# Kernel optimization log

Hardware: AMD Instinct MI355X
Metric: run time of the kernel (lower is better)

Reference implementation:

```python
import jax, jax.numpy as jnp
import numpy as np

DIM_MODEL = 1024
NUM_HEADS = 16
HEAD_DIM = DIM_MODEL // NUM_HEADS
NEG = -1000000000.0


def setup_inputs() -> dict:
    key = jax.random.key(0)
    ks = jax.random.split(key, 11)
    B, S, D = 2, 2048, DIM_MODEL
    s = 1.0 / np.sqrt(D)
    return {
        "q": jax.random.normal(ks[0], (B, S, D), jnp.float32),
        "k": jax.random.normal(ks[1], (B, S, D), jnp.float32),
        "v": jax.random.normal(ks[2], (B, S, D), jnp.float32),
        "Wq": jax.random.normal(ks[3], (D, D), jnp.float32) * s,
        "bq": jnp.zeros((D,), jnp.float32),
        "Wk": jax.random.normal(ks[4], (D, D), jnp.float32) * s,
        "bk": jnp.zeros((D,), jnp.float32),
        "Wv": jax.random.normal(ks[5], (D, D), jnp.float32) * s,
        "bv": jnp.zeros((D,), jnp.float32),
        "Wo": jax.random.normal(ks[6], (D, D), jnp.float32) * s,
        "bo": jnp.zeros((D,), jnp.float32),
    }


def reference(q, k, v, Wq, bq, Wk, bk, Wv, bv, Wo, bo):
    B, S, D = q.shape
    H, hd = NUM_HEADS, HEAD_DIM

    def proj(x, W, b):
        # torch Linear: x @ W.T + b, then split heads -> [B, H, S, hd]
        y = jnp.einsum("bsd,ed->bse", x, W) + b
        return y.reshape(B, S, H, hd).transpose(0, 2, 1, 3)

    qh = proj(q, Wq, bq)
    kh = proj(k, Wk, bk)
    vh = proj(v, Wv, bv)

    scores = jnp.einsum("bhqd,bhkd->bhqk", qh, kh) / np.sqrt(hd)
    # torch.triu(ones(S,S), diagonal=0): upper triangle INCLUDING diagonal is masked
    mask = jnp.triu(jnp.ones((S, S), bool))
    scores = jnp.where(mask, NEG, scores)
    # softmax over dim=-2 (query axis), as in the original module
    attn = jax.nn.softmax(scores, axis=-2)
    ctx = jnp.einsum("bhqk,bhkd->bhqd", attn, vh)  # [B,H,S,hd]
    ctx = ctx.transpose(0, 2, 1, 3).reshape(B, S, D)
    return jnp.einsum("bsd,ed->bse", ctx, Wo) + bo
```

## Files before the change

kernel.cpp:

```cpp
#include <hip/hip_runtime.h>

typedef __bf16 bf16;
typedef __attribute__((ext_vector_type(8))) __bf16 bf16x8;
typedef __attribute__((ext_vector_type(2))) __bf16 bf16x2;
typedef __attribute__((ext_vector_type(4))) float f32x4;

#define AS1 __attribute__((address_space(1)))
#define AS3 __attribute__((address_space(3)))

#define BB 2
#define SS 2048
#define DD 1024
#define HH 16
#define HD 64
#define BH (BB*HH)

#define QSCALE 0.1803368801111244f

static __device__ __forceinline__ f32x4 mfma16(bf16x8 a, bf16x8 b, f32x4 c) {
  return __builtin_amdgcn_mfma_f32_16x16x32_bf16(a, b, c, 0, 0, 0);
}
static __device__ __forceinline__ float fexp2(float x) {
  return __builtin_amdgcn_exp2f(x);
}

static __device__ __forceinline__ void swz1024(int bid, int& bh, int& a, int& b2) {
  int c = bid & 7, j = bid >> 3;
  bh = c + 8 * (j & 3);
  int rem = j >> 2;
  a = rem & 15;
  b2 = rem >> 4;
}

__global__ __launch_bounds__(256) void cvt_all(
    const float* __restrict__ w0, const float* __restrict__ w1,
    const float* __restrict__ w2, const float* __restrict__ w3,
    const float* __restrict__ x0, const float* __restrict__ x1, const float* __restrict__ x2,
    bf16* __restrict__ ow0, bf16* __restrict__ ow1, bf16* __restrict__ ow2,
    bf16* __restrict__ ow3, bf16* __restrict__ ox0, bf16* __restrict__ ox1,
    bf16* __restrict__ ox2) {
  const int z = blockIdx.y;
  const float* s;
  bf16* o;
  int n8;
  switch (z) {
    case 0: s = w0; o = ow0; n8 = 1024 * 1024 / 8; break;
    case 1: s = w1; o = ow1; n8 = 1024 * 1024 / 8; break;
    case 2: s = w2; o = ow2; n8 = 1024 * 1024 / 8; break;
    case 3: s = w3; o = ow3; n8 = 1024 * 1024 / 8; break;
    case 4: s = x0; o = ox0; n8 = 4096 * 1024 / 8; break;
    case 5: s = x1; o = ox1; n8 = 4096 * 1024 / 8; break;
    default: s = x2; o = ox2; n8 = 4096 * 1024 / 8; break;
  }
  int i = blockIdx.x * 256 + threadIdx.x;
  if (i >= n8) return;
  const float4* sp = (const float4*)s;
  float4 a = sp[2 * i], b = sp[2 * i + 1];
  bf16x8 v;
  v[0] = (bf16)a.x; v[1] = (bf16)a.y; v[2] = (bf16)a.z; v[3] = (bf16)a.w;
  v[4] = (bf16)b.x; v[5] = (bf16)b.y; v[6] = (bf16)b.z; v[7] = (bf16)b.w;
  ((bf16x8*)o)[i] = v;
}

__device__ __forceinline__ void gemm_core(const bf16* __restrict__ A,
                                          const bf16* __restrict__ Bm, int K,
                                          int m0, int n0, int w, int l,
                                          bf16* sA, bf16* sB, f32x4 (&acc)[4][4]) {
  const int l15 = l & 15, lg = l >> 4;
  const int wr = (w >> 1) * 64, wc = (w & 1) * 64;
  const int fv = (l15 >> 1) & 3;
  for (int kt = 0; kt < K; kt += 32) {
#pragma unroll
    for (int i = 0; i < 2; ++i) {
      int t = i * 256 + w * 64 + l;
      const int r = t >> 2, cs = (t & 3) ^ ((r >> 1) & 3);
      const bf16* ga = A + (size_t)(m0 + r) * K + kt + cs * 8;
      const bf16* gb = Bm + (size_t)(n0 + r) * K + kt + cs * 8;
      __builtin_amdgcn_global_load_lds((const AS1 void*)ga,
                                       (AS3 void*)(sA + (i * 256 + w * 64) * 8), 16, 0, 0);
      __builtin_amdgcn_global_load_lds((const AS1 void*)gb,
                                       (AS3 void*)(sB + (i * 256 + w * 64) * 8), 16, 0, 0);
    }
    __syncthreads();
    bf16x8 af[4], bfr[4];
#pragma unroll
    for (int m = 0; m < 4; ++m)
      af[m] = *(const bf16x8*)(sA + (wr + m * 16 + l15) * 32 + (lg ^ fv) * 8);
#pragma unroll
    for (int n = 0; n < 4; ++n)
      bfr[n] = *(const bf16x8*)(sB + (wc + n * 16 + l15) * 32 + (lg ^ fv) * 8);
#pragma unroll
    for (int m = 0; m < 4; ++m)
#pragma unroll
      for (int n = 0; n < 4; ++n)
        acc[m][n] = mfma16(af[m], bfr[n], acc[m][n]);
    __syncthreads();
  }
}

__global__ __launch_bounds__(256) void proj_gemm(
    const bf16* __restrict__ Xq, const bf16* __restrict__ Xk, const bf16* __restrict__ Xv,
    const bf16* __restrict__ Wq, const bf16* __restrict__ Wk, const bf16* __restrict__ Wv,
    const float* __restrict__ bq, const float* __restrict__ bk, const float* __restrict__ bv,
    bf16* __restrict__ Oq, bf16* __restrict__ Ok, bf16* __restrict__ Ovt) {
  __shared__ __align__(16) bf16 sA[128 * 32];
  __shared__ __align__(16) bf16 sB[128 * 32];
  const int bid = blockIdx.x;
  const int c = bid & 7, u = bid >> 3;
  const int mt = c * 4 + (u & 3);
  const int nt = (u >> 2) & 7;
  const int z = u >> 5;
  const bf16* A = (z == 0) ? Xq : ((z == 1) ? Xk : Xv);
  const bf16* W = (z == 0) ? Wq : ((z == 1) ? Wk : Wv);
  const float* bias = (z == 0) ? bq : ((z == 1) ? bk : bv);
  const int tid = threadIdx.x, l = tid & 63, w = tid >> 6;
  const int m0 = mt * 128, n0 = nt * 128;
  f32x4 acc[4][4] = {};
  gemm_core(A, W, DD, m0, n0, w, l, sA, sB, acc);
  const int l15 = l & 15, lg = l >> 4;
  const int wr = (w >> 1) * 64, wc = (w & 1) * 64;
#pragma unroll
  for (int n = 0; n < 4; ++n) {
    int col = n0 + wc + n * 16 + l15;
    float bb = bias[col];
    int h = col >> 6, d = col & 63;
#pragma unroll
    for (int m = 0; m < 4; ++m) {
#pragma unroll
      for (int r = 0; r < 4; ++r) {
        int row = m0 + wr + m * 16 + lg * 4 + r;
        int b = row >> 11, s = row & (SS - 1);
        float vv = acc[m][n][r] + bb;
        if (z == 0) vv *= QSCALE;
        if (z != 2)
          ((z == 0) ? Oq : Ok)[(((size_t)(b * HH + h)) * SS + s) * HD + d] = (bf16)vv;
        else
          Ovt[(size_t)(b * HH + h) * SS * HD + ((s >> 5) * 64 + d) * 32 + (s & 31)] = (bf16)vv;
      }
    }
  }
}

__global__ __launch_bounds__(256) void out_gemm(const bf16* __restrict__ A,
                                                const bf16* __restrict__ W,
                                                const float* __restrict__ bias,
                                                float* __restrict__ out) {
  __shared__ __align__(16) bf16 sA[128 * 32];
  __shared__ __align__(16) bf16 sB[128 * 32];
  const int bid = blockIdx.x;
  const int c = bid & 7, u = bid >> 3;
  const int mt = c * 4 + (u & 3);
  const int nt = (u >> 2) & 7;
  const int tid = threadIdx.x, l = tid & 63, w = tid >> 6;
  const int m0 = mt * 128, n0 = nt * 128;
  f32x4 acc[4][4] = {};
  gemm_core(A, W, DD, m0, n0, w, l, sA, sB, acc);
  const int l15 = l & 15, lg = l >> 4;
  const int wr = (w >> 1) * 64, wc = (w & 1) * 64;
#pragma unroll
  for (int n = 0; n < 4; ++n) {
    int col = n0 + wc + n * 16 + l15;
    float bb = bias[col];
#pragma unroll
    for (int m = 0; m < 4; ++m)
#pragma unroll
      for (int r = 0; r < 4; ++r) {
        int row = m0 + wr + m * 16 + lg * 4 + r;
        out[(size_t)row * DD + col] = acc[m][n][r] + bb;
      }
  }
}

__global__ __launch_bounds__(256) void colz(const bf16* __restrict__ Qb,
                                            const bf16* __restrict__ Kb,
                                            float* __restrict__ zPart) {
  __shared__ float zred[4][64];
  int bh, pair, qh;
  swz1024(blockIdx.x, bh, pair, qh);
  const int tid = threadIdx.x, l = tid & 63, w = tid >> 6;
  const int l15 = l & 15, lg = l >> 4;
  const bf16* Q = Qb + (size_t)bh * SS * HD;
  const bf16* Kh = Kb + (size_t)bh * SS * HD;

  for (int half = 0; half < 2; ++half) {
    const int s = half ? (31 - pair) : pair;
    const int c0 = s * 64;
    bf16x8 kf[4][2];
#pragma unroll
    for (int kt = 0; kt < 4; ++kt) {
      kf[kt][0] = *(const bf16x8*)&Kh[(c0 + kt * 16 + l15) * HD + lg * 8];
      kf[kt][1] = *(const bf16x8*)&Kh[(c0 + kt * 16 + l15) * HD + 32 + lg * 8];
    }
    float z[4] = {};
    const int qstart = c0 + qh * 64 + w * 16;
    bf16x8 qa0, qa1, qn0, qn1;
    if (qstart < SS) {
      qa0 = *(const bf16x8*)&Q[(qstart + l15) * HD + lg * 8];
      qa1 = *(const bf16x8*)&Q[(qstart + l15) * HD + 32 + lg * 8];
    }
    for (int qb = qstart; qb < SS; qb += 128) {
      const int qnext = qb + 128;
      if (qnext < SS) {
        qn0 = *(const bf16x8*)&Q[(qnext + l15) * HD + lg * 8];
        qn1 = *(const bf16x8*)&Q[(qnext + l15) * HD + 32 + lg * 8];
      }
      f32x4 d[4] = {};
#pragma unroll
      for (int kt = 0; kt < 4; ++kt) {
        d[kt] = mfma16(qa0, kf[kt][0], d[kt]);
        d[kt] = mfma16(qa1, kf[kt][1], d[kt]);
      }
#pragma unroll
      for (int kt = 0; kt < 4; ++kt) {
        const int kcol = c0 + kt * 16 + l15;
#pragma unroll
        for (int r = 0; r < 4; ++r) {
          int qq = qb + lg * 4 + r;
          z[kt] += (qq > kcol) ? fexp2(d[kt][r]) : 0.f;
        }
      }
      qa0 = qn0; qa1 = qn1;
    }
#pragma unroll
    for (int kt = 0; kt < 4; ++kt) {
      z[kt] += __shfl_xor(z[kt], 16);
      z[kt] += __shfl_xor(z[kt], 32);
    }
    if (l < 16) {
#pragma unroll
      for (int kt = 0; kt < 4; ++kt) zred[w][kt * 16 + l15] = z[kt];
    }
    __syncthreads();
    if (tid < 64) {
      float zs = zred[0][tid] + zred[1][tid] + zred[2][tid] + zred[3][tid];
      zPart[((size_t)qh * BH + bh) * SS + c0 + tid] = zs;
    }
    __syncthreads();
  }
}

__global__ __launch_bounds__(256) void vscale(bf16* __restrict__ Vt,
                                              const float* __restrict__ zPart,
                                              float* __restrict__ vlastB) {
  int i = blockIdx.x * 256 + threadIdx.x;
  int ks8 = i & 3;
  int d = (i >> 2) & 63;
  int ts = (i >> 8) & 63;
  int bh = i >> 14;
  bf16* p = Vt + ((((size_t)bh * 64 + ts) * 64 + d) * 32) + ks8 * 8;
  const float* z0 = zPart + (size_t)bh * SS + ts * 32 + ks8 * 8;
  const float* z1 = zPart + ((size_t)BH + bh) * SS + ts * 32 + ks8 * 8;
  bf16x8 v = *(const bf16x8*)p;
  if (ts == 63 && ks8 == 3) vlastB[bh * 64 + d] = (float)v[7] * (1.0f / (float)SS);
  f32x4 a0 = *(const f32x4*)z0, a1 = *(const f32x4*)(z0 + 4);
  f32x4 b0 = *(const f32x4*)z1, b1 = *(const f32x4*)(z1 + 4);
  f32x4 r0, r1;
#pragma unroll
  for (int j = 0; j < 4; ++j) {
    float s0 = a0[j] + b0[j], s1 = a1[j] + b1[j];
    r0[j] = (s0 > 0.f) ? 1.0f / s0 : 0.f;
    r1[j] = (s1 > 0.f) ? 1.0f / s1 : 0.f;
  }
  bf16x8 o;
#pragma unroll
  for (int j = 0; j < 4; ++j) o[j] = (bf16)((float)v[j] * r0[j]);
#pragma unroll
  for (int j = 0; j < 4; ++j) o[4 + j] = (bf16)((float)v[4 + j] * r1[j]);
  *(bf16x8*)p = o;
}

template <bool DIAG>
static __device__ __forceinline__ void chunk_compute(
    const bf16* sKe, const bf16* sVe, int k0, int qw,
    const bf16x8 (&qa)[2][2], f32x4 (&acc)[2][4], int l15, int lg) {
  const int fv = (l15 >> 1) & 3;
  const int slK = (lg ^ fv) * 8;
  bf16x8 kf00 = *(const bf16x8*)(sKe + l15 * 32 + slK);
  bf16x8 kf01 = *(const bf16x8*)(sKe + 1024 + l15 * 32 + slK);
  bf16x8 kf10 = *(const bf16x8*)(sKe + (16 + l15) * 32 + slK);
  bf16x8 kf11 = *(const bf16x8*)(sKe + 1024 + (16 + l15) * 32 + slK);
  union U { unsigned int u[4]; bf16x8 v; };
  U vf[4];
#pragma unroll
  for (int dt = 0; dt < 4; ++dt) {
    const bf16* base = sVe + (dt * 16 + l15) * 32;
    uint2 lo = *(const uint2*)&base[((lg >> 1) ^ fv) * 8 + (lg & 1) * 4];
    uint2 hi = *(const uint2*)&base[(((lg >> 1) + 2) ^ fv) * 8 + (lg & 1) * 4];
    vf[dt].u[0] = lo.x; vf[dt].u[1] = lo.y; vf[dt].u[2] = hi.x; vf[dt].u[3] = hi.y;
  }
  const int kb0i = k0 + lg * 4, kb1i = k0 + 16 + lg * 4;
#pragma unroll
  for (int qt = 0; qt < 2; ++qt) {
    f32x4 s0 = {}, s1 = {};
    s0 = mfma16(kf00, qa[qt][0], s0);
    s0 = mfma16(kf01, qa[qt][1], s0);
    s1 = mfma16(kf10, qa[qt][0], s1);
    s1 = mfma16(kf11, qa[qt][1], s1);
    const int qq = qw + qt * 16 + l15;
    U pa;
#pragma unroll
    for (int hw = 0; hw < 2; ++hw) {
      bf16x2 t0, t1;
#pragma unroll
      for (int r = 0; r < 2; ++r) {
        int rr = hw * 2 + r;
        float p0 = fexp2(s0[rr]);
        float p1 = fexp2(s1[rr]);
        if (DIAG) {
          p0 = (kb0i + rr < qq) ? p0 : 0.f;
          p1 = (kb1i + rr < qq) ? p1 : 0.f;
        }
        t0[r] = (bf16)p0;
        t1[r] = (bf16)p1;
      }
      pa.u[hw] = __builtin_bit_cast(unsigned int, t0);
      pa.u[hw + 2] = __builtin_bit_cast(unsigned int, t1);
    }
#pragma unroll
    for (int dt = 0; dt < 4; ++dt)
      acc[qt][dt] = mfma16(pa.v, vf[dt].v, acc[qt][dt]);
  }
}

__global__ __launch_bounds__(256, 2) void attn_ctx(const bf16* __restrict__ Qb,
                                                   const bf16* __restrict__ Kb,
                                                   const bf16* __restrict__ Vt,
                                                   bf16* __restrict__ P0,
                                                   bf16* __restrict__ P1,
                                                   bf16* __restrict__ P2,
                                                   bf16* __restrict__ P3) {
  __shared__ __align__(16) bf16 sK[2 * 32 * 32];
  __shared__ __align__(16) bf16 sV[64 * 32];
  int bh, a, b2;
  swz1024(blockIdx.x, bh, a, b2);
  const int pr = a & 7;
  const int j = (b2 << 1) | (a >> 3);
  const int tid = threadIdx.x, l = tid & 63, w = tid >> 6;
  const int l15 = l & 15, lg = l >> 4;
  const bf16* Q = Qb + (size_t)bh * SS * HD;
  const bf16* Kh = Kb + (size_t)bh * SS * HD;
  const bf16* V = Vt + (size_t)bh * SS * HD;
  bf16* ctxP = (j == 0) ? P0 : (j == 1) ? P1 : (j == 2) ? P2 : P3;
  const int b = bh >> 4, h = bh & 15;

  const int skk = tid >> 7, sr = (tid >> 2) & 31, sc = tid & 3;
  const int scs = sc ^ ((sr >> 1) & 3);
  const int vr = tid >> 2;
  const int vcs = (tid & 3) ^ ((vr >> 1) & 3);
  bf16* dK = sK + (size_t)w * 512;
  bf16* dV = sV + (size_t)w * 512;

  for (int half = 0; half < 2; ++half) {
    const int T = half ? (15 - pr) : pr;
    const int q0 = T * 128;
    const int qw = q0 + w * 32;

    bf16x8 qa[2][2];
#pragma unroll
    for (int qt = 0; qt < 2; ++qt)
#pragma unroll
      for (int kk = 0; kk < 2; ++kk)
        qa[qt][kk] = *(const bf16x8*)&Q[(qw + qt * 16 + l15) * HD + kk * 32 + lg * 8];

    f32x4 acc[2][4] = {};
    const int kend = q0 + 128;
    for (int k0 = j * 32; k0 < kend; k0 += 128) {
      const bf16* gK = Kh + (size_t)(k0 + sr) * HD + skk * 32 + scs * 8;
      const bf16* gV = V + (((size_t)(k0 >> 5)) << 11) + vr * 32 + vcs * 8;
      __builtin_amdgcn_global_load_lds((const AS1 void*)gK, (AS3 void*)dK, 16, 0, 0);
      __builtin_amdgcn_global_load_lds((const AS1 void*)gV, (AS3 void*)dV, 16, 0, 0);
      __syncthreads();
      if (k0 < qw)
        chunk_compute<false>(sK, sV, k0, qw, qa, acc, l15, lg);
      else if (k0 == qw)
        chunk_compute<true>(sK, sV, k0, qw, qa, acc, l15, lg);
      __syncthreads();
    }

#pragma unroll
    for (int qt = 0; qt < 2; ++qt)
#pragma unroll
      for (int r = 0; r < 4; ++r) {
        int q = qw + qt * 16 + lg * 4 + r;
#pragma unroll
        for (int dt = 0; dt < 4; ++dt)
          ctxP[((size_t)(b * SS + q)) * DD + h * HD + dt * 16 + l15] =
              (bf16)acc[qt][dt][r];
      }
  }
}

__global__ __launch_bounds__(256) void ctxfin(const bf16* __restrict__ P1,
                                              const bf16* __restrict__ P2,
                                              const bf16* __restrict__ P3,
                                              const float* __restrict__ vlastB,
                                              bf16* __restrict__ ctx) {
  int i = blockIdx.x * 256 + threadIdx.x;
  int e0 = i * 8;
  int row = e0 >> 10, col = e0 & (DD - 1);
  int b = row >> 11;
  int vidx = (b * HH + (col >> 6)) * 64 + (col & 63);
  bf16x8 p0 = ((const bf16x8*)ctx)[i];
  bf16x8 p1 = ((const bf16x8*)P1)[i];
  bf16x8 p2 = ((const bf16x8*)P2)[i];
  bf16x8 p3 = ((const bf16x8*)P3)[i];
  f32x4 v0 = *(const f32x4*)&vlastB[vidx];
  f32x4 v1 = *(const f32x4*)&vlastB[vidx + 4];
  bf16x8 o;
#pragma unroll
  for (int jj = 0; jj < 4; ++jj)
    o[jj] = (bf16)(((float)p0[jj] + (float)p1[jj]) + ((float)p2[jj] + (float)p3[jj]) + v0[jj]);
#pragma unroll
  for (int jj = 0; jj < 4; ++jj)
    o[4 + jj] = (bf16)(((float)p0[4 + jj] + (float)p1[4 + jj]) +
                       ((float)p2[4 + jj] + (float)p3[4 + jj]) + v1[jj]);
  ((bf16x8*)ctx)[i] = o;
}

extern "C" void kernel_launch(void* const* d_in, const int* in_sizes, int n_in,
                              void* d_out, int out_size, void* d_ws, size_t ws_size,
                              hipStream_t stream) {
  const float* q  = (const float*)d_in[0];
  const float* k  = (const float*)d_in[1];
  const float* v  = (const float*)d_in[2];
  const float* Wq = (const float*)d_in[3];
  const float* bq = (const float*)d_in[4];
  const float* Wk = (const float*)d_in[5];
  const float* bk = (const float*)d_in[6];
  const float* Wv = (const float*)d_in[7];
  const float* bv = (const float*)d_in[8];
  const float* Wo = (const float*)d_in[9];
  const float* bo = (const float*)d_in[10];

  char* ws = (char*)d_ws;
  const size_t SZP = (size_t)4096 * 1024 * 2;
  const size_t SZW = (size_t)1024 * 1024 * 2;
  bf16* Qb   = (bf16*)(ws + 0 * SZP);
  bf16* Kb   = (bf16*)(ws + 1 * SZP);
  bf16* Vt   = (bf16*)(ws + 2 * SZP);
  bf16* ctxb = (bf16*)(ws + 3 * SZP);
  bf16* qb16 = (bf16*)(ws + 4 * SZP);
  bf16* kb16 = (bf16*)(ws + 5 * SZP);
  bf16* vb16 = (bf16*)(ws + 6 * SZP);
  bf16* Wqb  = (bf16*)(ws + 7 * SZP + 0 * SZW);
  bf16* Wkb  = (bf16*)(ws + 7 * SZP + 1 * SZW);
  bf16* Wvb  = (bf16*)(ws + 7 * SZP + 2 * SZW);
  bf16* Wob  = (bf16*)(ws + 7 * SZP + 3 * SZW);
  float* zPart = (float*)(ws + 7 * SZP + 4 * SZW);
  float* vlastB = zPart + (size_t)2 * BH * SS;

  cvt_all<<<dim3(2048, 7), 256, 0, stream>>>(Wq, Wk, Wv, Wo, q, k, v,
                                             Wqb, Wkb, Wvb, Wob, qb16, kb16, vb16);

  proj_gemm<<<768, 256, 0, stream>>>(
      qb16, kb16, vb16, Wqb, Wkb, Wvb, bq, bk, bv, Qb, Kb, Vt);

  colz<<<1024, 256, 0, stream>>>(Qb, Kb, zPart);
  vscale<<<(BH * HD * SS / 8) / 256, 256, 0, stream>>>(Vt, zPart, vlastB);
  attn_ctx<<<1024, 256, 0, stream>>>(Qb, Kb, Vt, ctxb, qb16, kb16, vb16);
  ctxfin<<<(4096 * 1024 / 8) / 256, 256, 0, stream>>>(qb16, kb16, vb16, vlastB, ctxb);

  out_gemm<<<256, 256, 0, stream>>>(ctxb, Wob, bo, (float*)d_out);
}
```

Measured before the change: 144.5 us.

## Fuse fp32-to-bf16 activation conversion into projection GEMM tile loads

The separate pass that converted the q/k/v activations to bf16 is removed. The projection GEMM now loads fp32 activation tiles straight into LDS using a swizzled layout and converts them to bf16 while reading fragments. Only the weights are still converted by a smaller standalone kernel. This avoids writing and re-reading three 8 MB bf16 copies, but doubles the LDS traffic and footprint for the A tile and adds conversion instructions inside the GEMM inner loop.

Measured after the change: 141.5 us, median of 2. -2.0%, faster.

```diff
diff --git a/kernel.cpp b/kernel.cpp
--- a/kernel.cpp
+++ b/kernel.cpp
@@ -32,34 +32,101 @@
   b2 = rem >> 4;
 }
 
-__global__ __launch_bounds__(256) void cvt_all(
-    const float* __restrict__ w0, const float* __restrict__ w1,
-    const float* __restrict__ w2, const float* __restrict__ w3,
-    const float* __restrict__ x0, const float* __restrict__ x1, const float* __restrict__ x2,
-    bf16* __restrict__ ow0, bf16* __restrict__ ow1, bf16* __restrict__ ow2,
-    bf16* __restrict__ ow3, bf16* __restrict__ ox0, bf16* __restrict__ ox1,
-    bf16* __restrict__ ox2) {
+__global__ __launch_bounds__(256) void cvt_w(const float* __restrict__ s0, const float* __restrict__ s1,
+                                             const float* __restrict__ s2, const float* __restrict__ s3,
+                                             bf16* __restrict__ o0, bf16* __restrict__ o1,
+                                             bf16* __restrict__ o2, bf16* __restrict__ o3) {
   const int z = blockIdx.y;
-  const float* s;
-  bf16* o;
-  int n8;
-  switch (z) {
-    case 0: s = w0; o = ow0; n8 = 1024 * 1024 / 8; break;
-    case 1: s = w1; o = ow1; n8 = 1024 * 1024 / 8; break;
-    case 2: s = w2; o = ow2; n8 = 1024 * 1024 / 8; break;
-    case 3: s = w3; o = ow3; n8 = 1024 * 1024 / 8; break;
-    case 4: s = x0; o = ox0; n8 = 4096 * 1024 / 8; break;
-    case 5: s = x1; o = ox1; n8 = 4096 * 1024 / 8; break;
-    default: s = x2; o = ox2; n8 = 4096 * 1024 / 8; break;
-  }
+  const float* s = (z == 0) ? s0 : (z == 1) ? s1 : (z == 2) ? s2 : s3;
+  bf16* o = (z == 0) ? o0 : (z == 1) ? o1 : (z == 2) ? o2 : o3;
   int i = blockIdx.x * 256 + threadIdx.x;
-  if (i >= n8) return;
   const float4* sp = (const float4*)s;
   float4 a = sp[2 * i], b = sp[2 * i + 1];
   bf16x8 v;
   v[0] = (bf16)a.x; v[1] = (bf16)a.y; v[2] = (bf16)a.z; v[3] = (bf16)a.w;
   v[4] = (bf16)b.x; v[5] = (bf16)b.y; v[6] = (bf16)b.z; v[7] = (bf16)b.w;
   ((bf16x8*)o)[i] = v;
+}
+
+__global__ __launch_bounds__(256) void proj_gemm(
+    const float* __restrict__ Xq, const float* __restrict__ Xk, const float* __restrict__ Xv,
+    const bf16* __restrict__ Wq, const bf16* __restrict__ Wk, const bf16* __restrict__ Wv,
+    const float* __restrict__ bq, const float* __restrict__ bk, const float* __restrict__ bv,
+    bf16* __restrict__ Oq, bf16* __restrict__ Ok, bf16* __restrict__ Ovt) {
+  __shared__ __align__(16) float sA[128 * 32];
+  __shared__ __align__(16) bf16 sB[128 * 32];
+  const int bid = blockIdx.x;
+  const int c = bid & 7, u = bid >> 3;
+  const int mt = c * 4 + (u & 3);
+  const int nt = (u >> 2) & 7;
+  const int z = u >> 5;
+  const float* X = (z == 0) ? Xq : ((z == 1) ? Xk : Xv);
+  const bf16* W = (z == 0) ? Wq : ((z == 1) ? Wk : Wv);
+  const float* bias = (z == 0) ? bq : ((z == 1) ? bk : bv);
+  const int tid = threadIdx.x, l = tid & 63, w = tid >> 6;
+  const int m0 = mt * 128, n0 = nt * 128;
+  const int l15 = l & 15, lg = l >> 4;
+  const int wr = (w >> 1) * 64, wc = (w & 1) * 64;
+  const int fB = (l15 >> 1) & 3;
+  const int fA = l15 & 7;
+  f32x4 acc[4][4] = {};
+  for (int kt = 0; kt < DD; kt += 32) {
+#pragma unroll
+    for (int i = 0; i < 4; ++i) {
+      int s = i * 256 + tid;
+      int r = s >> 3, cs = (s & 7) ^ (r & 7);
+      const float* ga = X + (size_t)(m0 + r) * DD + kt + cs * 4;
+      __builtin_amdgcn_global_load_lds((const AS1 void*)ga, (AS3 void*)(sA + s * 4), 16, 0, 0);
+    }
+#pragma unroll
+    for (int i = 0; i < 2; ++i) {
+      int t = i * 256 + tid;
+      int r = t >> 2, cs = (t & 3) ^ ((r >> 1) & 3);
+      const bf16* gb = W + (size_t)(n0 + r) * DD + kt + cs * 8;
+      __builtin_amdgcn_global_load_lds((const AS1 void*)gb, (AS3 void*)(sB + t * 8), 16, 0, 0);
+    }
+    __syncthreads();
+    bf16x8 af[4], bfr[4];
+#pragma unroll
+    for (int m = 0; m < 4; ++m) {
+      const float* base = sA + (wr + m * 16 + l15) * 32;
+      f32x4 u0 = *(const f32x4*)(base + (((2 * lg) ^ fA) << 2));
+      f32x4 u1 = *(const f32x4*)(base + (((2 * lg + 1) ^ fA) << 2));
+      bf16x8 o;
+      o[0] = (bf16)u0[0]; o[1] = (bf16)u0[1]; o[2] = (bf16)u0[2]; o[3] = (bf16)u0[3];
+      o[4] = (bf16)u1[0]; o[5] = (bf16)u1[1]; o[6] = (bf16)u1[2]; o[7] = (bf16)u1[3];
+      af[m] = o;
+    }
+#pragma unroll
+    for (int n = 0; n < 4; ++n)
+      bfr[n] = *(const bf16x8*)(sB + (wc + n * 16 + l15) * 32 + (lg ^ fB) * 8);
+#pragma unroll
+    for (int m = 0; m < 4; ++m)
+#pragma unroll
+      for (int n = 0; n < 4; ++n)
+        acc[m][n] = mfma16(af[m], bfr[n], acc[m][n]);
+    __syncthreads();
+  }
+#pragma unroll
+  for (int n = 0; n < 4; ++n) {
+    int col = n0 + wc + n * 16 + l15;
+    float bb = bias[col];
+    int h = col >> 6, d = col & 63;
+#pragma unroll
+    for (int m = 0; m < 4; ++m) {
+#pragma unroll
+      for (int r = 0; r < 4; ++r) {
+        int row = m0 + wr + m * 16 + lg * 4 + r;
+        int b = row >> 11, s = row & (SS - 1);
+        float vv = acc[m][n][r] + bb;
+        if (z == 0) vv *= QSCALE;
+        if (z != 2)
+          ((z == 0) ? Oq : Ok)[(((size_t)(b * HH + h)) * SS + s) * HD + d] = (bf16)vv;
+        else
+          Ovt[(size_t)(b * HH + h) * SS * HD + ((s >> 5) * 64 + d) * 32 + (s & 31)] = (bf16)vv;
+      }
+    }
+  }
 }
 
 __device__ __forceinline__ void gemm_core(const bf16* __restrict__ A,
@@ -95,49 +162,6 @@
       for (int n = 0; n < 4; ++n)
         acc[m][n] = mfma16(af[m], bfr[n], acc[m][n]);
     __syncthreads();
-  }
-}
-
-__global__ __launch_bounds__(256) void proj_gemm(
-    const bf16* __restrict__ Xq, const bf16* __restrict__ Xk, const bf16* __restrict__ Xv,
-    const bf16* __restrict__ Wq, const bf16* __restrict__ Wk, const bf16* __restrict__ Wv,
-    const float* __restrict__ bq, const float* __restrict__ bk, const float* __restrict__ bv,
-    bf16* __restrict__ Oq, bf16* __restrict__ Ok, bf16* __restrict__ Ovt) {
-  __shared__ __align__(16) bf16 sA[128 * 32];
-  __shared__ __align__(16) bf16 sB[128 * 32];
-  const int bid = blockIdx.x;
-  const int c = bid & 7, u = bid >> 3;
-  const int mt = c * 4 + (u & 3);
-  const int nt = (u >> 2) & 7;
-  const int z = u >> 5;
-  const bf16* A = (z == 0) ? Xq : ((z == 1) ? Xk : Xv);
-  const bf16* W = (z == 0) ? Wq : ((z == 1) ? Wk : Wv);
-  const float* bias = (z == 0) ? bq : ((z == 1) ? bk : bv);
-  const int tid = threadIdx.x, l = tid & 63, w = tid >> 6;
-  const int m0 = mt * 128, n0 = nt * 128;
-  f32x4 acc[4][4] = {};
-  gemm_core(A, W, DD, m0, n0, w, l, sA, sB, acc);
-  const int l15 = l & 15, lg = l >> 4;
-  const int wr = (w >> 1) * 64, wc = (w & 1) * 64;
-#pragma unroll
-  for (int n = 0; n < 4; ++n) {
-    int col = n0 + wc + n * 16 + l15;
-    float bb = bias[col];
-    int h = col >> 6, d = col & 63;
-#pragma unroll
-    for (int m = 0; m < 4; ++m) {
-#pragma unroll
-      for (int r = 0; r < 4; ++r) {
-        int row = m0 + wr + m * 16 + lg * 4 + r;
-        int b = row >> 11, s = row & (SS - 1);
-        float vv = acc[m][n][r] + bb;
-        if (z == 0) vv *= QSCALE;
-        if (z != 2)
-          ((z == 0) ? Oq : Ok)[(((size_t)(b * HH + h)) * SS + s) * HD + d] = (bf16)vv;
-        else
-          Ovt[(size_t)(b * HH + h) * SS * HD + ((s >> 5) * 64 + d) * 32 + (s & 31)] = (bf16)vv;
-      }
-    }
   }
 }
 
@@ -439,9 +463,9 @@
   bf16* Kb   = (bf16*)(ws + 1 * SZP);
   bf16* Vt   = (bf16*)(ws + 2 * SZP);
   bf16* ctxb = (bf16*)(ws + 3 * SZP);
-  bf16* qb16 = (bf16*)(ws + 4 * SZP);
-  bf16* kb16 = (bf16*)(ws + 5 * SZP);
-  bf16* vb16 = (bf16*)(ws + 6 * SZP);
+  bf16* P1   = (bf16*)(ws + 4 * SZP);
+  bf16* P2   = (bf16*)(ws + 5 * SZP);
+  bf16* P3   = (bf16*)(ws + 6 * SZP);
   bf16* Wqb  = (bf16*)(ws + 7 * SZP + 0 * SZW);
   bf16* Wkb  = (bf16*)(ws + 7 * SZP + 1 * SZW);
   bf16* Wvb  = (bf16*)(ws + 7 * SZP + 2 * SZW);
@@ -449,16 +473,15 @@
   float* zPart = (float*)(ws + 7 * SZP + 4 * SZW);
   float* vlastB = zPart + (size_t)2 * BH * SS;
 
-  cvt_all<<<dim3(2048, 7), 256, 0, stream>>>(Wq, Wk, Wv, Wo, q, k, v,
-                                             Wqb, Wkb, Wvb, Wob, qb16, kb16, vb16);
+  cvt_w<<<dim3(512, 4), 256, 0, stream>>>(Wq, Wk, Wv, Wo, Wqb, Wkb, Wvb, Wob);
 
   proj_gemm<<<768, 256, 0, stream>>>(
-      qb16, kb16, vb16, Wqb, Wkb, Wvb, bq, bk, bv, Qb, Kb, Vt);
+      q, k, v, Wqb, Wkb, Wvb, bq, bk, bv, Qb, Kb, Vt);
 
   colz<<<1024, 256, 0, stream>>>(Qb, Kb, zPart);
   vscale<<<(BH * HD * SS / 8) / 256, 256, 0, stream>>>(Vt, zPart, vlastB);
-  attn_ctx<<<1024, 256, 0, stream>>>(Qb, Kb, Vt, ctxb, qb16, kb16, vb16);
-  ctxfin<<<(4096 * 1024 / 8) / 256, 256, 0, stream>>>(qb16, kb16, vb16, vlastB, ctxb);
+  attn_ctx<<<1024, 256, 0, stream>>>(Qb, Kb, Vt, ctxb, P1, P2, P3);
+  ctxfin<<<(4096 * 1024 / 8) / 256, 256, 0, stream>>>(P1, P2, P3, vlastB, ctxb);
 
   out_gemm<<<256, 256, 0, stream>>>(ctxb, Wob, bo, (float*)d_out);
 }
```
